# Performance work log

Measured on AMD Instinct MI355X. Metric: run time of the kernel, lower is better.

The kernel has to match this reference:

```python
import jax, jax.numpy as jnp
import numpy as np

B, S, D, H = 4, 1024, 1024, 16
DK = D // H
MASK_WEIGHT_0 = 1.0   # weight for key-type 0 (from (weight, mask_mat) tuple)
MASK_WEIGHT_1 = 0.5   # weight for key-type 1
NEG_INF = -1.0e9


def setup_inputs() -> dict:
    key = jax.random.key(0)
    ks = jax.random.split(key, 10)
    wscale = 0.02
    return {
        "query": jax.random.normal(ks[0], (B, S, D), jnp.float32),
        "key_x": jax.random.normal(ks[1], (B, S, D), jnp.float32),
        "value": jax.random.normal(ks[2], (B, S, D), jnp.float32),
        "mask0": jax.random.randint(ks[3], (B, S, S), 0, 2, jnp.int32),
        "mask1": jax.random.randint(ks[4], (B, S, S), 0, 2, jnp.int32),
        "Wq":  wscale * jax.random.normal(ks[5], (D, D), jnp.float32),
        "Wk0": wscale * jax.random.normal(ks[6], (D, D), jnp.float32),
        "Wk1": wscale * jax.random.normal(ks[7], (D, D), jnp.float32),
        "Wv":  wscale * jax.random.normal(ks[8], (D, D), jnp.float32),
        "Wo":  wscale * jax.random.normal(ks[9], (D, D), jnp.float32),
    }


def _heads(x, W):
    # torch nn.Linear: x @ W.T ; then view(B,S,H,DK).transpose(1,2)
    return (x @ W.T).reshape(B, S, H, DK).transpose(0, 2, 1, 3)  # [B,H,S,DK]


def reference(query, key_x, value, mask0, mask1, Wq, Wk0, Wk1, Wv, Wo):
    q = _heads(query, Wq)          # [B,H,S,DK]
    k0 = _heads(key_x, Wk0)
    k1 = _heads(key_x, Wk1)
    v = _heads(value, Wv)
    scale = 1.0 / jnp.sqrt(jnp.float32(DK))

    def masked_score(k, mask, weight):
        s = jnp.einsum('bhqd,bhkd->bhqk', q, k) * scale       # [B,H,S,S]
        keep = (mask != 0)[:, None, :, :]                     # broadcast over heads
        # (score * weight*keep).masked_fill(mask==0, -1e9)
        return jnp.where(keep, s * weight, NEG_INF)

    scores = masked_score(k0, mask0, MASK_WEIGHT_0) + masked_score(k1, mask1, MASK_WEIGHT_1)
    p_attn = jax.nn.sigmoid(scores)                           # activation='sigmoid'
    x = jnp.einsum('bhqk,bhkd->bhqd', p_attn, v)              # [B,H,S,DK]
    x = x.transpose(0, 2, 1, 3).reshape(B, S, D)
    return x @ Wo.T                                            # output_linear (dropout p=0)
```

## Files before the change

kernel.cpp:

```cpp
#include <hip/hip_runtime.h>

#define B_  4
#define S_  1024
#define D_  1024
#define H_  16
#define DK_ 64

typedef __attribute__((ext_vector_type(8)))  short bf16x8;
typedef __attribute__((ext_vector_type(4)))  short bf16x4;
typedef __attribute__((ext_vector_type(4)))  float f32x4;
typedef __attribute__((ext_vector_type(16))) float f32x16;

static __device__ __forceinline__ unsigned short f2bf(float f) {
  union { float f; unsigned u; } v; v.f = f;
  unsigned r = v.u + 0x7FFFu + ((v.u >> 16) & 1u);
  return (unsigned short)(r >> 16);
}

static __device__ __forceinline__ unsigned cvtpk(float lo, float hi) {
  unsigned r;
  asm("v_cvt_pk_bf16_f32 %0, %1, %2" : "=v"(r) : "v"(lo), "v"(hi));
  return r;
}
static __device__ __forceinline__ void plswap(unsigned &a, unsigned &b) {
  asm volatile("v_permlane32_swap_b32 %0, %1" : "+v"(a), "+v"(b));
}

typedef __attribute__((address_space(1))) const void gc_t;
typedef __attribute__((address_space(3))) void lds_t;
static __device__ __forceinline__ void gload_lds16(const void* g, void* l) {
  __builtin_amdgcn_global_load_lds((gc_t*)g, (lds_t*)l, 16, 0, 0);
}

#define TM_ (1u << 22)
#define WM_ (1u << 20)

#define CEXP_ (-0.18033688011112042f)

__global__ __launch_bounds__(256)
void prep(const float* __restrict__ w0, const float* __restrict__ w1,
          const float* __restrict__ w2, const float* __restrict__ w3,
          const float* __restrict__ w4, unsigned short* __restrict__ wbf)
{
  const size_t u = ((size_t)blockIdx.x * 256 + threadIdx.x) * 16;
  const int seg = (int)(u >> 20);
  const size_t off = u & (WM_ - 1);
  unsigned short t[16];
  unsigned short* dst = wbf + (size_t)seg * WM_ + off;
  if (seg == 1) {
    float4 a[4], b[4];
#pragma unroll
    for (int i = 0; i < 4; ++i) a[i] = *(const float4*)(w1 + off + 4*i);
#pragma unroll
    for (int i = 0; i < 4; ++i) b[i] = *(const float4*)(w2 + off + 4*i);
#pragma unroll
    for (int i = 0; i < 4; ++i) {
      t[4*i]   = f2bf(a[i].x + 0.5f*b[i].x);
      t[4*i+1] = f2bf(a[i].y + 0.5f*b[i].y);
      t[4*i+2] = f2bf(a[i].z + 0.5f*b[i].z);
      t[4*i+3] = f2bf(a[i].w + 0.5f*b[i].w);
    }
  } else {
    const float sc = (seg == 0) ? CEXP_ : 1.0f;
    const float* src = (seg == 0) ? w0 : (seg == 2 ? w3 : w4);
    float4 f[4];
#pragma unroll
    for (int i = 0; i < 4; ++i) f[i] = *(const float4*)(src + off + 4*i);
#pragma unroll
    for (int i = 0; i < 4; ++i) {
      t[4*i]   = f2bf(sc*f[i].x); t[4*i+1] = f2bf(sc*f[i].y);
      t[4*i+2] = f2bf(sc*f[i].z); t[4*i+3] = f2bf(sc*f[i].w);
    }
  }
  *(bf16x8*)dst       = *(bf16x8*)&t[0];
  *(bf16x8*)(dst + 8) = *(bf16x8*)&t[8];
}

__global__ __launch_bounds__(256, 4)
void proj_gemm(const float* __restrict__ qx, const float* __restrict__ kx,
               const float* __restrict__ vx,
               const unsigned short* __restrict__ wbf,
               unsigned short* __restrict__ Qb, unsigned short* __restrict__ Kh,
               unsigned short* __restrict__ Vth,
               const int* __restrict__ ma, const int* __restrict__ mb,
               unsigned long long* __restrict__ pk)
{
  __shared__ unsigned short As[128][64];
  __shared__ unsigned short Ws[128][64];

  const int tid = threadIdx.x, bid = blockIdx.x;

  if (bid >= 768) {
    const int row = bid - 768;
    const int w4  = tid >> 6, lw = tid & 63;
    const int4 a  = *(const int4*)(ma + (size_t)row*1024 + w4*256 + lw*4);
    const int4 b  = *(const int4*)(mb + (size_t)row*1024 + w4*256 + lw*4);
    const unsigned long long b0 = __ballot((a.x != 0) & (b.x != 0));
    const unsigned long long b1 = __ballot((a.y != 0) & (b.y != 0));
    const unsigned long long b2 = __ballot((a.z != 0) & (b.z != 0));
    const unsigned long long b3 = __ballot((a.w != 0) & (b.w != 0));
    if (lw < 4) {
      const unsigned long long wv =
            ((b0 >> (16*lw)) & 0xFFFFull)
         | (((b1 >> (16*lw)) & 0xFFFFull) << 16)
         | (((b2 >> (16*lw)) & 0xFFFFull) << 32)
         | (((b3 >> (16*lw)) & 0xFFFFull) << 48);
      pk[(size_t)row*16 + w4*4 + lw] = wv;
    }
    return;
  }

  const int xcd = bid & 7, c = bid >> 3;
  const int L = xcd * 96 + c;
  const int which = L >> 8;
  const int rem = L & 255;
  const int nt = rem >> 5, mt = rem & 31;
  const int m0 = mt * 128, n0 = nt * 128;
  const int w = tid >> 6, l = tid & 63;
  const int lr = l & 15, lg = l >> 4;
  const int wr = w >> 1, wc = w & 1;

  const float* Af = (which == 0) ? qx : (which == 1) ? kx : vx;
  const unsigned short* W = wbf + (size_t)which * WM_;

  const f32x4 fzero = {0.f, 0.f, 0.f, 0.f};
  f32x4 acc[4][4];
#pragma unroll
  for (int m = 0; m < 4; m++)
#pragma unroll
    for (int n = 0; n < 4; n++) acc[m][n] = fzero;

  const int r0  = tid >> 3;
  const int cg  = tid & 7;
  const int aswz = (cg ^ (r0 & 7)) * 8;
  const float* aSrc = Af + (size_t)(m0 + r0) * 1024 + cg * 8;

  const int srow8 = l >> 3;
  const int sg    = ((l & 7) ^ srow8) * 8;
  const unsigned short* wBase = W + (size_t)(n0 + w*32 + srow8) * 1024 + sg;

  const int rc0 = ((lg)     ^ (lr & 7)) * 8;
  const int rc1 = ((4 + lg) ^ (lr & 7)) * 8;

  for (int kk = 0; kk < 1024; kk += 64) {
    float4 fa[4][2];
#pragma unroll
    for (int p = 0; p < 4; ++p) {
      const float* s = aSrc + (size_t)(p*32) * 1024 + kk;
      fa[p][0] = *(const float4*)s;
      fa[p][1] = *(const float4*)(s + 4);
    }
#pragma unroll
    for (int cc = 0; cc < 4; ++cc)
      gload_lds16(wBase + (size_t)cc * 8 * 1024 + kk, &Ws[w*32 + cc*8][0]);
#pragma unroll
    for (int p = 0; p < 4; ++p) {
      union { unsigned u[4]; bf16x8 v; } pu;
      pu.u[0] = cvtpk(fa[p][0].x, fa[p][0].y);
      pu.u[1] = cvtpk(fa[p][0].z, fa[p][0].w);
      pu.u[2] = cvtpk(fa[p][1].x, fa[p][1].y);
      pu.u[3] = cvtpk(fa[p][1].z, fa[p][1].w);
      *(bf16x8*)&As[p*32 + r0][aswz] = pu.v;
    }
    __syncthreads();

#pragma unroll
    for (int ks = 0; ks < 2; ++ks) {
      const int rc = ks ? rc1 : rc0;
      bf16x8 af[4], bfr[4];
#pragma unroll
      for (int m = 0; m < 4; m++) af[m]  = *(const bf16x8*)&As[wr*64 + m*16 + lr][rc];
#pragma unroll
      for (int n = 0; n < 4; n++) bfr[n] = *(const bf16x8*)&Ws[wc*64 + n*16 + lr][rc];
#pragma unroll
      for (int m = 0; m < 4; m++)
#pragma unroll
        for (int n = 0; n < 4; n++)
          acc[m][n] = __builtin_amdgcn_mfma_f32_16x16x32_bf16(af[m], bfr[n], acc[m][n], 0, 0, 0);
    }
    __syncthreads();
  }

  if (which == 2) {
#pragma unroll
    for (int m = 0; m < 4; m++) {
      const int row = m0 + wr*64 + m*16 + lg*4;
      const int b = row >> 10, s = row & 1023;
#pragma unroll
      for (int n = 0; n < 4; n++) {
        const int col = n0 + wc*64 + n*16 + lr;
        const int h = col >> 6, dk = col & 63;
        unsigned short tv[4] = {f2bf(acc[m][n][0]), f2bf(acc[m][n][1]),
                                f2bf(acc[m][n][2]), f2bf(acc[m][n][3])};
        const size_t a = ((size_t)((b*H_ + h)*DK_ + dk)) * S_
                       + (size_t)(s & ~63) + ((((s >> 3) & 7) ^ (dk & 7)) << 3) + (s & 7);
        *(bf16x4*)(Vth + a) = *(bf16x4*)tv;
      }
    }
  } else if (which == 0) {
#pragma unroll
    for (int m = 0; m < 4; m++) {
      const int row = m0 + wr*64 + m*16 + lg*4;
#pragma unroll
      for (int n = 0; n < 4; n++) {
        const int col = n0 + wc*64 + n*16 + lr;
#pragma unroll
        for (int r = 0; r < 4; r++)
          Qb[(size_t)(row + r) * 1024 + col] = f2bf(acc[m][n][r]);
      }
    }
  } else {
#pragma unroll
    for (int m = 0; m < 4; m++) {
      const int row = m0 + wr*64 + m*16 + lg*4;
#pragma unroll
      for (int n = 0; n < 4; n++) {
        const int col = n0 + wc*64 + n*16 + lr;
        const int h = col >> 6, dk = col & 63;
#pragma unroll
        for (int r = 0; r < 4; r++) {
          const int rr = row + r;
          const int b = rr >> 10, s = rr & 1023;
          const size_t a = ((size_t)((b*H_ + h)*S_ + s)) * 64
                         + (((dk >> 3) ^ (s & 7)) << 3) + (dk & 7);
          Kh[a] = f2bf(acc[m][n][r]);
        }
      }
    }
  }
}

__global__ __launch_bounds__(256, 4)
void out_gemm(const unsigned short* __restrict__ A,
              const unsigned short* __restrict__ W, float* __restrict__ C)
{
  __shared__ unsigned short As[128][64];
  __shared__ unsigned short Ws2[64][64];

  const int tid = threadIdx.x, bid = blockIdx.x;
  const int xcd = bid & 7, idx = bid >> 3;
  const int mt = (xcd << 2) | (idx & 3);
  const int nt = idx >> 2;
  const int m0 = mt * 128, n0 = nt * 64;
  const int w = tid >> 6, l = tid & 63;
  const int lr = l & 15, lg = l >> 4;
  const int wr = w >> 1, wc = w & 1;

  const f32x4 fzero = {0.f, 0.f, 0.f, 0.f};
  f32x4 acc[4][2];
#pragma unroll
  for (int m = 0; m < 4; m++)
#pragma unroll
    for (int n = 0; n < 2; n++) acc[m][n] = fzero;

  const int srow8 = l >> 3;
  const int sg    = ((l & 7) ^ srow8) * 8;
  const int rc0 = ((lg)     ^ (lr & 7)) * 8;
  const int rc1 = ((4 + lg) ^ (lr & 7)) * 8;

  const unsigned short* aBase = A + (size_t)(m0 + w*32 + srow8) * 1024 + sg;
  const unsigned short* wBase = W + (size_t)(n0 + w*16 + srow8) * 1024 + sg;

  for (int kk = 0; kk < 1024; kk += 64) {
#pragma unroll
    for (int cc = 0; cc < 4; ++cc)
      gload_lds16(aBase + (size_t)cc * 8 * 1024 + kk, &As[w*32 + cc*8][0]);
#pragma unroll
    for (int cc = 0; cc < 2; ++cc)
      gload_lds16(wBase + (size_t)cc * 8 * 1024 + kk, &Ws2[w*16 + cc*8][0]);
    __syncthreads();

#pragma unroll
    for (int ks = 0; ks < 2; ++ks) {
      const int rc = ks ? rc1 : rc0;
      bf16x8 af[4], bfr[2];
#pragma unroll
      for (int m = 0; m < 4; m++) af[m]  = *(const bf16x8*)&As[wr*64 + m*16 + lr][rc];
#pragma unroll
      for (int n = 0; n < 2; n++) bfr[n] = *(const bf16x8*)&Ws2[wc*32 + n*16 + lr][rc];
#pragma unroll
      for (int m = 0; m < 4; m++)
#pragma unroll
        for (int n = 0; n < 2; n++)
          acc[m][n] = __builtin_amdgcn_mfma_f32_16x16x32_bf16(af[m], bfr[n], acc[m][n], 0, 0, 0);
    }
    __syncthreads();
  }

#pragma unroll
  for (int m = 0; m < 4; m++) {
    const int row = m0 + wr*64 + m*16 + lg*4;
#pragma unroll
    for (int n = 0; n < 2; n++) {
      const int col = n0 + wc*32 + n*16 + lr;
#pragma unroll
      for (int r = 0; r < 4; r++)
        C[(size_t)(row + r) * 1024 + col] = acc[m][n][r];
    }
  }
}

__global__ __launch_bounds__(512)
void attn_kernel(const unsigned short* __restrict__ Q,
                 const unsigned short* __restrict__ Kh,
                 const unsigned short* __restrict__ Vth,
                 const unsigned long long* __restrict__ mpk,
                 unsigned short* __restrict__ X)
{
  __shared__ unsigned short Ks[2][2][4096];
  __shared__ unsigned short Vs[2][2][4096];

  const int tid  = threadIdx.x;
  const int bid0 = blockIdx.x;
  const int bid = ((bid0 & 7) << 6) | (bid0 >> 3);
  const int qt = bid & 7, h = (bid >> 3) & 15, b = bid >> 7;
  const int q0 = qt * 128;
  const int w8 = tid >> 6, lw = tid & 63;
  const int grp = w8 >> 2, qw = w8 & 3;
  const int l31 = lw & 31, hh = lw >> 5, l7 = lw & 7;
  const int bh = b * H_ + h;

  bf16x8 qf[4];
  {
    const unsigned short* qp = Q + ((size_t)(b*S_ + q0 + qw*32 + l31)) * D_ + h*DK_ + hh*8;
#pragma unroll
    for (int ds = 0; ds < 4; ++ds) qf[ds] = *(const bf16x8*)(qp + ds*16);
  }
  const size_t mbase = ((size_t)(b*S_ + q0 + qw*32 + l31)) * 16 + grp*8;

  f32x16 acc0, acc1;
#pragma unroll
  for (int r = 0; r < 16; ++r) { acc0[r] = 0.f; acc1[r] = 0.f; }

  const unsigned short* gp[4];
  unsigned short* lb[4];
  int stp[4];
#pragma unroll
  for (int c = 0; c < 4; ++c) {
    const int e = qw*4 + c;
    const int bu = e >> 3, s = e & 7;
    lb[c] = (bu == 0 ? &Ks[grp][0][0] : &Vs[grp][0][0]) + s*512;
    if (bu == 0) {
      gp[c]  = Kh + (size_t)bh * 65536 + grp*32768 + s*512 + lw*8;
      stp[c] = 4096;
    } else {
      gp[c]  = Vth + ((size_t)(bh*DK_ + s*8 + (lw >> 3))) * S_ + grp*512 + (lw & 7) * 8;
      stp[c] = 64;
    }
  }

#define STAGE(nxt)                                                     \
  {                                                                    \
    _Pragma("unroll")                                                  \
    for (int c = 0; c < 4; ++c) {                                      \
      gload_lds16(gp[c], lb[c] + (nxt)*4096);                          \
      gp[c] += stp[c];                                                 \
    }                                                                  \
  }

  STAGE(0);
  __syncthreads();
  unsigned long long mw = mpk[mbase];
  int cur = 0;

  for (int t = 0; t < 8; ++t) {
    unsigned long long mw_n = 0;
    if (t < 7) { STAGE(cur ^ 1); mw_n = mpk[mbase + t + 1]; }

#pragma unroll
    for (int sub = 0; sub < 2; ++sub) {
      const int rbase = (sub*32 + l31) * 64;
      f32x16 sv;
#pragma unroll
      for (int r = 0; r < 16; ++r) sv[r] = 0.f;
      __builtin_amdgcn_s_setprio(1);
#pragma unroll
      for (int ds = 0; ds < 4; ++ds) {
        const int g = (((ds*2 + hh) ^ l7)) * 8;
        const bf16x8 kf = *(const bf16x8*)&Ks[grp][cur][rbase + g];
        sv = __builtin_amdgcn_mfma_f32_32x32x16_bf16(kf, qf[ds], sv, 0, 0, 0);
      }
      __builtin_amdgcn_s_setprio(0);

      const unsigned long long ams = mw >> (8*sub + hh);
      float p[16];
#pragma unroll
      for (int r = 0; r < 16; ++r) {
        const int cbit = 16*(r & 3) + 2*(r >> 2);
        const float e  = __builtin_amdgcn_exp2f(sv[r]);
        const float pr = __builtin_amdgcn_rcpf(1.0f + e);
        p[r] = ((ams >> cbit) & 1ull) ? pr : 0.f;
      }

      bf16x8 pa[2];
#pragma unroll
      for (int ks = 0; ks < 2; ++ks) {
        const int a0 = ks*8;
        unsigned u0 = cvtpk(p[a0+0], p[a0+1]);
        unsigned u1 = cvtpk(p[a0+2], p[a0+3]);
        unsigned u2 = cvtpk(p[a0+4], p[a0+5]);
        unsigned u3 = cvtpk(p[a0+6], p[a0+7]);
        plswap(u0, u2);
        plswap(u1, u3);
        union { unsigned u[4]; bf16x8 v; } pu;
        pu.u[0] = u0; pu.u[1] = u1; pu.u[2] = u2; pu.u[3] = u3;
        pa[ks] = pu.v;
      }

      __builtin_amdgcn_s_setprio(1);
#pragma unroll
      for (int ks = 0; ks < 2; ++ks) {
        const int g = ((sub*4 + ks*2 + hh) ^ l7) * 8;
        const bf16x8 vb0 = *(const bf16x8*)&Vs[grp][cur][(l31)      * 64 + g];
        const bf16x8 vb1 = *(const bf16x8*)&Vs[grp][cur][(32 + l31) * 64 + g];
        acc0 = __builtin_amdgcn_mfma_f32_32x32x16_bf16(pa[ks], vb0, acc0, 0, 0, 0);
        acc1 = __builtin_amdgcn_mfma_f32_32x32x16_bf16(pa[ks], vb1, acc1, 0, 0, 0);
      }
      __builtin_amdgcn_s_setprio(0);
    }

    if (t < 7) {
      __syncthreads();
      mw = mw_n;
      cur ^= 1;
    }
  }
#undef STAGE

  __syncthreads();
  float2* cmb = (float2*)&Ks[0][0][0];
  if (grp == 1) {
#pragma unroll
    for (int i = 0; i < 8; ++i)
      cmb[(qw*16 + i)*64 + lw] = make_float2(acc0[2*i], acc0[2*i+1]);
#pragma unroll
    for (int i = 0; i < 8; ++i)
      cmb[(qw*16 + 8 + i)*64 + lw] = make_float2(acc1[2*i], acc1[2*i+1]);
  }
  __syncthreads();
  if (grp == 0) {
#pragma unroll
    for (int i = 0; i < 8; ++i) {
      float2 v = cmb[(qw*16 + i)*64 + lw];
      acc0[2*i] += v.x; acc0[2*i+1] += v.y;
    }
#pragma unroll
    for (int i = 0; i < 8; ++i) {
      float2 v = cmb[(qw*16 + 8 + i)*64 + lw];
      acc1[2*i] += v.x; acc1[2*i+1] += v.y;
    }
#pragma unroll
    for (int r = 0; r < 16; ++r) {
      const int qrow = q0 + qw*32 + (r & 3) + 8*(r >> 2) + 4*hh;
      unsigned short* xp = X + ((size_t)(b*S_ + qrow)) * D_ + h*DK_ + l31;
      xp[0]  = f2bf(acc0[r]);
      xp[32] = f2bf(acc1[r]);
    }
  }
}

extern "C" void kernel_launch(void* const* d_in, const int* in_sizes, int n_in,
                              void* d_out, int out_size, void* d_ws, size_t ws_size,
                              hipStream_t stream)
{
  const float* query = (const float*)d_in[0];
  const float* key_x = (const float*)d_in[1];
  const float* value = (const float*)d_in[2];
  const int*   mask0 = (const int*)d_in[3];
  const int*   mask1 = (const int*)d_in[4];
  const float* Wq    = (const float*)d_in[5];
  const float* Wk0   = (const float*)d_in[6];
  const float* Wk1   = (const float*)d_in[7];
  const float* Wv    = (const float*)d_in[8];
  const float* Wo    = (const float*)d_in[9];

  unsigned short* ws = (unsigned short*)d_ws;
  unsigned short* Xb  = ws;
  unsigned short* wbf = ws + (size_t)3 * TM_;
  unsigned short* Qb  = ws + (size_t)3 * TM_ + 4 * WM_;
  unsigned short* Kh  = Qb  + (size_t)TM_;
  unsigned short* Vth = Kh  + (size_t)TM_;
  unsigned long long* mpk = (unsigned long long*)(Vth + (size_t)TM_);

  prep<<<dim3(1024), dim3(256), 0, stream>>>(Wq, Wk0, Wk1, Wv, Wo, wbf);

  proj_gemm<<<dim3(768 + 4096), dim3(256), 0, stream>>>(
      query, key_x, value, wbf, Qb, Kh, Vth, mask0, mask1, mpk);

  attn_kernel<<<dim3(B_ * H_ * (S_ / 128)), dim3(512), 0, stream>>>(
      Qb, Kh, Vth, mpk, Xb);

  out_gemm<<<dim3(512), dim3(256), 0, stream>>>(Xb, wbf + (size_t)3 * WM_,
                                                (float*)d_out);
}
```

Before: 111.3 us.

## Double-buffer projection GEMM K-loop and move mask packing into prep kernel

The projection GEMM now double-buffers its A and W LDS tiles. It prefetches the next K slice from global memory while MFMAs run on the current one, raises wave priority around the MFMA block, and needs only one barrier per iteration. Occupancy hint drops from 4 to 2 blocks per CU because LDS doubles. The mask bit-packing blocks move out of proj_gemm into the prep kernel, so the GEMM launch holds only the 768 GEMM tiles.

Result: slower. 123.9 us (+11.3%).

```diff
diff --git a/kernel.cpp b/kernel.cpp
--- a/kernel.cpp
+++ b/kernel.cpp
@@ -40,59 +40,46 @@
 __global__ __launch_bounds__(256)
 void prep(const float* __restrict__ w0, const float* __restrict__ w1,
           const float* __restrict__ w2, const float* __restrict__ w3,
-          const float* __restrict__ w4, unsigned short* __restrict__ wbf)
+          const float* __restrict__ w4, unsigned short* __restrict__ wbf,
+          const int* __restrict__ ma, const int* __restrict__ mb,
+          unsigned long long* __restrict__ pk)
 {
-  const size_t u = ((size_t)blockIdx.x * 256 + threadIdx.x) * 16;
-  const int seg = (int)(u >> 20);
-  const size_t off = u & (WM_ - 1);
-  unsigned short t[16];
-  unsigned short* dst = wbf + (size_t)seg * WM_ + off;
-  if (seg == 1) {
-    float4 a[4], b[4];
-#pragma unroll
-    for (int i = 0; i < 4; ++i) a[i] = *(const float4*)(w1 + off + 4*i);
-#pragma unroll
-    for (int i = 0; i < 4; ++i) b[i] = *(const float4*)(w2 + off + 4*i);
-#pragma unroll
-    for (int i = 0; i < 4; ++i) {
-      t[4*i]   = f2bf(a[i].x + 0.5f*b[i].x);
-      t[4*i+1] = f2bf(a[i].y + 0.5f*b[i].y);
-      t[4*i+2] = f2bf(a[i].z + 0.5f*b[i].z);
-      t[4*i+3] = f2bf(a[i].w + 0.5f*b[i].w);
-    }
+  if (blockIdx.x < 1024) {
+    const size_t u = ((size_t)blockIdx.x * 256 + threadIdx.x) * 16;
+    const int seg = (int)(u >> 20);
+    const size_t off = u & (WM_ - 1);
+    unsigned short t[16];
+    unsigned short* dst = wbf + (size_t)seg * WM_ + off;
+    if (seg == 1) {
+      float4 a[4], b[4];
+#pragma unroll
+      for (int i = 0; i < 4; ++i) a[i] = *(const float4*)(w1 + off + 4*i);
+#pragma unroll
+      for (int i = 0; i < 4; ++i) b[i] = *(const float4*)(w2 + off + 4*i);
+#pragma unroll
+      for (int i = 0; i < 4; ++i) {
+        t[4*i]   = f2bf(a[i].x + 0.5f*b[i].x);
+        t[4*i+1] = f2bf(a[i].y + 0.5f*b[i].y);
+        t[4*i+2] = f2bf(a[i].z + 0.5f*b[i].z);
+        t[4*i+3] = f2bf(a[i].w + 0.5f*b[i].w);
+      }
+    } else {
+      const float sc = (seg == 0) ? CEXP_ : 1.0f;
+      const float* src = (seg == 0) ? w0 : (seg == 2 ? w3 : w4);
+      float4 f[4];
+#pragma unroll
+      for (int i = 0; i < 4; ++i) f[i] = *(const float4*)(src + off + 4*i);
+#pragma unroll
+      for (int i = 0; i < 4; ++i) {
+        t[4*i]   = f2bf(sc*f[i].x); t[4*i+1] = f2bf(sc*f[i].y);
+        t[4*i+2] = f2bf(sc*f[i].z); t[4*i+3] = f2bf(sc*f[i].w);
+      }
+    }
+    *(bf16x8*)dst       = *(bf16x8*)&t[0];
+    *(bf16x8*)(dst + 8) = *(bf16x8*)&t[8];
   } else {
-    const float sc = (seg == 0) ? CEXP_ : 1.0f;
-    const float* src = (seg == 0) ? w0 : (seg == 2 ? w3 : w4);
-    float4 f[4];
-#pragma unroll
-    for (int i = 0; i < 4; ++i) f[i] = *(const float4*)(src + off + 4*i);
-#pragma unroll
-    for (int i = 0; i < 4; ++i) {
-      t[4*i]   = f2bf(sc*f[i].x); t[4*i+1] = f2bf(sc*f[i].y);
-      t[4*i+2] = f2bf(sc*f[i].z); t[4*i+3] = f2bf(sc*f[i].w);
-    }
-  }
-  *(bf16x8*)dst       = *(bf16x8*)&t[0];
-  *(bf16x8*)(dst + 8) = *(bf16x8*)&t[8];
-}
-
-__global__ __launch_bounds__(256, 4)
-void proj_gemm(const float* __restrict__ qx, const float* __restrict__ kx,
-               const float* __restrict__ vx,
-               const unsigned short* __restrict__ wbf,
-               unsigned short* __restrict__ Qb, unsigned short* __restrict__ Kh,
-               unsigned short* __restrict__ Vth,
-               const int* __restrict__ ma, const int* __restrict__ mb,
-               unsigned long long* __restrict__ pk)
-{
-  __shared__ unsigned short As[128][64];
-  __shared__ unsigned short Ws[128][64];
-
-  const int tid = threadIdx.x, bid = blockIdx.x;
-
-  if (bid >= 768) {
-    const int row = bid - 768;
-    const int w4  = tid >> 6, lw = tid & 63;
+    const int row = blockIdx.x - 1024;
+    const int w4  = threadIdx.x >> 6, lw = threadIdx.x & 63;
     const int4 a  = *(const int4*)(ma + (size_t)row*1024 + w4*256 + lw*4);
     const int4 b  = *(const int4*)(mb + (size_t)row*1024 + w4*256 + lw*4);
     const unsigned long long b0 = __ballot((a.x != 0) & (b.x != 0));
@@ -107,9 +94,20 @@
          | (((b3 >> (16*lw)) & 0xFFFFull) << 48);
       pk[(size_t)row*16 + w4*4 + lw] = wv;
     }
-    return;
-  }
-
+  }
+}
+
+__global__ __launch_bounds__(256, 2)
+void proj_gemm(const float* __restrict__ qx, const float* __restrict__ kx,
+               const float* __restrict__ vx,
+               const unsigned short* __restrict__ wbf,
+               unsigned short* __restrict__ Qb, unsigned short* __restrict__ Kh,
+               unsigned short* __restrict__ Vth)
+{
+  __shared__ unsigned short As[2][128][64];
+  __shared__ unsigned short Ws[2][128][64];
+
+  const int tid = threadIdx.x, bid = blockIdx.x;
   const int xcd = bid & 7, c = bid >> 3;
   const int L = xcd * 96 + c;
   const int which = L >> 8;
@@ -142,44 +140,64 @@
   const int rc0 = ((lg)     ^ (lr & 7)) * 8;
   const int rc1 = ((4 + lg) ^ (lr & 7)) * 8;
 
-  for (int kk = 0; kk < 1024; kk += 64) {
-    float4 fa[4][2];
-#pragma unroll
-    for (int p = 0; p < 4; ++p) {
-      const float* s = aSrc + (size_t)(p*32) * 1024 + kk;
-      fa[p][0] = *(const float4*)s;
-      fa[p][1] = *(const float4*)(s + 4);
-    }
-#pragma unroll
-    for (int cc = 0; cc < 4; ++cc)
-      gload_lds16(wBase + (size_t)cc * 8 * 1024 + kk, &Ws[w*32 + cc*8][0]);
-#pragma unroll
-    for (int p = 0; p < 4; ++p) {
-      union { unsigned u[4]; bf16x8 v; } pu;
-      pu.u[0] = cvtpk(fa[p][0].x, fa[p][0].y);
-      pu.u[1] = cvtpk(fa[p][0].z, fa[p][0].w);
-      pu.u[2] = cvtpk(fa[p][1].x, fa[p][1].y);
-      pu.u[3] = cvtpk(fa[p][1].z, fa[p][1].w);
-      *(bf16x8*)&As[p*32 + r0][aswz] = pu.v;
-    }
-    __syncthreads();
-
+  float4 fa[4][2];
+#define LOADA(kk)                                                        \
+  { _Pragma("unroll")                                                    \
+    for (int p = 0; p < 4; ++p) {                                        \
+      const float* s_ = aSrc + (size_t)(p*32) * 1024 + (kk);             \
+      fa[p][0] = *(const float4*)s_;                                     \
+      fa[p][1] = *(const float4*)(s_ + 4);                               \
+    } }
+#define CVTWRITE(buf)                                                    \
+  { _Pragma("unroll")                                                    \
+    for (int p = 0; p < 4; ++p) {                                        \
+      union { unsigned u[4]; bf16x8 v; } pu_;                            \
+      pu_.u[0] = cvtpk(fa[p][0].x, fa[p][0].y);                          \
+      pu_.u[1] = cvtpk(fa[p][0].z, fa[p][0].w);                          \
+      pu_.u[2] = cvtpk(fa[p][1].x, fa[p][1].y);                          \
+      pu_.u[3] = cvtpk(fa[p][1].z, fa[p][1].w);                          \
+      *(bf16x8*)&As[buf][p*32 + r0][aswz] = pu_.v;                       \
+    } }
+#define LOADW(kk, buf)                                                   \
+  { _Pragma("unroll")                                                    \
+    for (int cc = 0; cc < 4; ++cc)                                       \
+      gload_lds16(wBase + (size_t)cc * 8 * 1024 + (kk),                  \
+                  &Ws[buf][w*32 + cc*8][0]); }
+
+  LOADA(0); CVTWRITE(0); LOADW(0, 0);
+  __syncthreads();
+  int cur = 0;
+
+  for (int t = 0; t < 16; ++t) {
+    const int kk1 = (t + 1) * 64;
+    if (t < 15) { LOADA(kk1); LOADW(kk1, cur ^ 1); }
+
+    __builtin_amdgcn_s_setprio(1);
 #pragma unroll
     for (int ks = 0; ks < 2; ++ks) {
       const int rc = ks ? rc1 : rc0;
       bf16x8 af[4], bfr[4];
 #pragma unroll
-      for (int m = 0; m < 4; m++) af[m]  = *(const bf16x8*)&As[wr*64 + m*16 + lr][rc];
-#pragma unroll
-      for (int n = 0; n < 4; n++) bfr[n] = *(const bf16x8*)&Ws[wc*64 + n*16 + lr][rc];
+      for (int m = 0; m < 4; m++) af[m]  = *(const bf16x8*)&As[cur][wr*64 + m*16 + lr][rc];
+#pragma unroll
+      for (int n = 0; n < 4; n++) bfr[n] = *(const bf16x8*)&Ws[cur][wc*64 + n*16 + lr][rc];
 #pragma unroll
       for (int m = 0; m < 4; m++)
 #pragma unroll
         for (int n = 0; n < 4; n++)
           acc[m][n] = __builtin_amdgcn_mfma_f32_16x16x32_bf16(af[m], bfr[n], acc[m][n], 0, 0, 0);
     }
-    __syncthreads();
-  }
+    __builtin_amdgcn_s_setprio(0);
+
+    if (t < 15) {
+      CVTWRITE(cur ^ 1);
+      __syncthreads();
+      cur ^= 1;
+    }
+  }
+#undef LOADA
+#undef CVTWRITE
+#undef LOADW
 
   if (which == 2) {
 #pragma unroll
@@ -482,10 +500,11 @@
   unsigned short* Vth = Kh  + (size_t)TM_;
   unsigned long long* mpk = (unsigned long long*)(Vth + (size_t)TM_);
 
-  prep<<<dim3(1024), dim3(256), 0, stream>>>(Wq, Wk0, Wk1, Wv, Wo, wbf);
-
-  proj_gemm<<<dim3(768 + 4096), dim3(256), 0, stream>>>(
-      query, key_x, value, wbf, Qb, Kh, Vth, mask0, mask1, mpk);
+  prep<<<dim3(1024 + 4096), dim3(256), 0, stream>>>(
+      Wq, Wk0, Wk1, Wv, Wo, wbf, mask0, mask1, mpk);
+
+  proj_gemm<<<dim3(768), dim3(256), 0, stream>>>(
+      query, key_x, value, wbf, Qb, Kh, Vth);
 
   attn_kernel<<<dim3(B_ * H_ * (S_ / 128)), dim3(512), 0, stream>>>(
       Qb, Kh, Vth, mpk, Xb);
```
